# Kernel tuning notes

Measured on AMD Instinct MI355X. Metric: run time of the kernel, lower is better.

## Reference

```python
import jax, jax.numpy as jnp
import numpy as np


def setup_inputs() -> dict:
    key = jax.random.key(0)
    ks = jax.random.split(key, 4)
    B, T, I, H = 64, 1024, 256, 512
    s = 1.0 / np.sqrt(I + H)  # torch Linear default init scale
    xs = jax.random.normal(ks[0], (B, T, I), dtype=jnp.float32)
    Wz = jax.random.uniform(ks[1], (I + H, H), jnp.float32, -s, s)
    Wr = jax.random.uniform(ks[2], (I + H, H), jnp.float32, -s, s)
    Wh = jax.random.uniform(ks[3], (I + H, H), jnp.float32, -s, s)
    bz = jnp.zeros((H,), jnp.float32)
    br = jnp.zeros((H,), jnp.float32)
    bh = jnp.zeros((H,), jnp.float32)
    return {"xs": xs, "Wz": Wz, "bz": bz, "Wr": Wr, "br": br, "Wh": Wh, "bh": bh}


def reference(xs, Wz, bz, Wr, br, Wh, bh):
    B, T, I = xs.shape
    H = Wz.shape[1]
    # split weights into input / hidden blocks so per-step work avoids concat
    Wz_x, Wz_h = Wz[:I], Wz[I:]
    Wr_x, Wr_h = Wr[:I], Wr[I:]
    Wh_x, Wh_h = Wh[:I], Wh[I:]
    # precompute all input projections in one big GEMM per gate: [B,T,H]
    xz = jnp.einsum('bti,ih->bth', xs, Wz_x) + bz
    xr = jnp.einsum('bti,ih->bth', xs, Wr_x) + br
    xh = jnp.einsum('bti,ih->bth', xs, Wh_x) + bh

    def step(h, inp):
        xz_t, xr_t, xh_t = inp
        zt = jax.nn.sigmoid(xz_t + h @ Wz_h)
        rt = jax.nn.sigmoid(xr_t + h @ Wr_h)
        ht = jnp.tanh(xh_t + (rt * h) @ Wh_h)
        h_next = (1 - zt) * h + zt * ht
        return h_next, h_next

    h0 = jnp.zeros((B, H), xs.dtype)
    # scan over time: inputs as [T, B, H]
    xs_t = (jnp.swapaxes(xz, 0, 1), jnp.swapaxes(xr, 0, 1), jnp.swapaxes(xh, 0, 1))
    h_last, hs = jax.lax.scan(step, h0, xs_t)
    return jnp.swapaxes(hs, 0, 1), h_last
```

## Files before the change

### kernel.cpp

```cpp
#include <hip/hip_runtime.h>
#include <cmath>

typedef __bf16 bf16x8 __attribute__((ext_vector_type(8)));
typedef float  f32x4  __attribute__((ext_vector_type(4)));
typedef unsigned int u32;
typedef unsigned long long u64;
typedef u32 u32x4v __attribute__((ext_vector_type(4)));

#define T_STEPS 1024
#define I_DIM   256
#define H_DIM   512
#define B_TOT   64
#define NBT     4
#define NCT     32
#define BT      16
#define CT      16
#define FDOM    64
#define WPB     (H_DIM / 2)
#define LLSZ    (2 * NBT * BT * WPB)

__device__ __forceinline__ f32x4 mfma16(bf16x8 a, bf16x8 b, f32x4 c) {
    return __builtin_amdgcn_mfma_f32_16x16x32_bf16(a, b, c, 0, 0, 0);
}

__device__ __forceinline__ bf16x8 cvt8r(float4 a, float4 b) {
    bf16x8 f;
    f[0] = (__bf16)a.x; f[1] = (__bf16)a.y; f[2] = (__bf16)a.z; f[3] = (__bf16)a.w;
    f[4] = (__bf16)b.x; f[5] = (__bf16)b.y; f[6] = (__bf16)b.z; f[7] = (__bf16)b.w;
    return f;
}

__device__ __forceinline__ int ld_flag(const int* p) {
    return __hip_atomic_load(p, __ATOMIC_RELAXED, __HIP_MEMORY_SCOPE_AGENT);
}
__device__ __forceinline__ void st_flag(int* p, int v) {
    __hip_atomic_store(p, v, __ATOMIC_RELAXED, __HIP_MEMORY_SCOPE_AGENT);
}
__device__ __forceinline__ u64 ld_u64(const u64* p) {
    return __hip_atomic_load(p, __ATOMIC_RELAXED, __HIP_MEMORY_SCOPE_AGENT);
}
__device__ __forceinline__ void st_u64(u64* p, u64 v) {
    __hip_atomic_store(p, v, __ATOMIC_RELAXED, __HIP_MEMORY_SCOPE_AGENT);
}

__device__ __forceinline__ void wait32(const int* fdom, int target) {
    const int* p = fdom + (threadIdx.x & 31);
    for (int g = 0; g < (1 << 22); ++g) {
        int v = ld_flag(p);
        if (__ballot(v >= target) == ~0ull) break;
    }
    asm volatile("" ::: "memory");
}

__device__ __forceinline__ void ll_load16(const u64* b0, const u64* b1,
                                          const u64* b2, const u64* b3,
                                          u32 tag, u64* wrd) {
    for (int g = 0; g < (1 << 20); ++g) {
        #pragma unroll
        for (int k = 0; k < 4; ++k) {
            wrd[0  + k] = ld_u64(b0 + k);
            wrd[4  + k] = ld_u64(b1 + k);
            wrd[8  + k] = ld_u64(b2 + k);
            wrd[12 + k] = ld_u64(b3 + k);
        }
        bool ok = true;
        #pragma unroll
        for (int x = 0; x < 16; ++x) ok &= ((u32)(wrd[x] >> 32) == tag);
        if (__ballot(ok) == ~0ull) break;
        __builtin_amdgcn_s_sleep(2);
    }
}

__device__ __forceinline__ bf16x8 frag_of(const u64* wrd) {
    u32x4v d;
    d.x = (u32)wrd[0]; d.y = (u32)wrd[1]; d.z = (u32)wrd[2]; d.w = (u32)wrd[3];
    return __builtin_bit_cast(bf16x8, d);
}

__global__ __launch_bounds__(256, 1) void gru_persist(
    const float* __restrict__ xs,
    const float* __restrict__ Wz, const float* __restrict__ bz,
    const float* __restrict__ Wr, const float* __restrict__ br,
    const float* __restrict__ Wh, const float* __restrict__ bh,
    float* __restrict__ out,
    u64* hll, u64* rhll, int* flag_h, int* flag_r)
{
    const int bid  = blockIdx.x;
    const int i    = bid & (NBT - 1);
    const int j    = bid >> 2;
    const int tid  = threadIdx.x;
    const int w    = tid >> 6;
    const int lane = tid & 63;
    const int q    = lane >> 4;
    const int ln   = lane & 15;
    const int cb   = j * CT;

    __shared__ float red1[2][4][16][17];
    __shared__ float red2[4][16][17];

    bf16x8 BZ[6], BR[6], BH[6];
    #pragma unroll
    for (int s = 0; s < 6; ++s) {
        int kk = w + 4 * s;
        int krow = kk * 32 + q * 8;
        bf16x8 fz, fr, fh;
        #pragma unroll
        for (int jj = 0; jj < 8; ++jj) {
            int off = (krow + jj) * H_DIM + cb + ln;
            fz[jj] = (__bf16)Wz[off];
            fr[jj] = (__bf16)Wr[off];
            fh[jj] = (__bf16)Wh[off];
        }
        BZ[s] = fz; BR[s] = fr; BH[s] = fh;
    }

    const int m = tid >> 4;
    const int c = tid & 15;
    const float bzc = bz[cb + c], brc = br[cb + c], bhc = bh[cb + c];
    float hprev = 0.0f;

    const float* xrow = xs + (size_t)(i * BT + ln) * T_STEPS * I_DIM;
    int* fh_dom = flag_h + i * FDOM;
    int* fr_dom = flag_r + i * FDOM;
    int* my_fh  = fh_dom + j;
    int* my_fr  = fr_dom + j;

    const int widx = q * 4;

    float4 xr[4];
    {
        const float* x0 = xrow;
        xr[0] = *(const float4*)(x0 + (w    ) * 32 + q * 8);
        xr[1] = *(const float4*)(x0 + (w    ) * 32 + q * 8 + 4);
        xr[2] = *(const float4*)(x0 + (w + 4) * 32 + q * 8);
        xr[3] = *(const float4*)(x0 + (w + 4) * 32 + q * 8 + 4);
    }

    for (int t = 0; t < T_STEPS; ++t) {
        const int p = t & 1, pp = p ^ 1;

        float4 xn[4];
        {
            int tn = (t + 1 < T_STEPS) ? t + 1 : t;
            const float* xp = xrow + (size_t)tn * I_DIM;
            xn[0] = *(const float4*)(xp + (w    ) * 32 + q * 8);
            xn[1] = *(const float4*)(xp + (w    ) * 32 + q * 8 + 4);
            xn[2] = *(const float4*)(xp + (w + 4) * 32 + q * 8);
            xn[3] = *(const float4*)(xp + (w + 4) * 32 + q * 8 + 4);
        }

        f32x4 accz = {0,0,0,0}, accr = {0,0,0,0}, acch = {0,0,0,0};

        {
            bf16x8 ax0 = cvt8r(xr[0], xr[1]);
            bf16x8 ax1 = cvt8r(xr[2], xr[3]);
            accz = mfma16(ax0, BZ[0], accz);
            accr = mfma16(ax0, BR[0], accr);
            acch = mfma16(ax0, BH[0], acch);
            accz = mfma16(ax1, BZ[1], accz);
            accr = mfma16(ax1, BR[1], accr);
            acch = mfma16(ax1, BH[1], acch);
        }

        {
            if (t > 0) wait32(fh_dom, t);
            const u64* hb = hll + ((size_t)((pp * NBT + i) * BT) + ln) * WPB;
            u64 wh[16];
            ll_load16(hb + (w     ) * 16 + widx,
                      hb + (w +  4) * 16 + widx,
                      hb + (w +  8) * 16 + widx,
                      hb + (w + 12) * 16 + widx,
                      (u32)t, wh);
            #pragma unroll
            for (int s = 0; s < 4; ++s) {
                bf16x8 ah = frag_of(&wh[4 * s]);
                accz = mfma16(ah, BZ[s + 2], accz);
                accr = mfma16(ah, BR[s + 2], accr);
            }
        }

        #pragma unroll
        for (int r4 = 0; r4 < 4; ++r4) {
            red1[0][w][q*4 + r4][ln] = accz[r4];
            red1[1][w][q*4 + r4][ln] = accr[r4];
        }
        __syncthreads();

        float zv;
        {
            float pz = red1[0][0][m][c] + red1[0][1][m][c] + red1[0][2][m][c] + red1[0][3][m][c] + bzc;
            float pr = red1[1][0][m][c] + red1[1][1][m][c] + red1[1][2][m][c] + red1[1][3][m][c] + brc;
            zv = 1.0f / (1.0f + __expf(-pz));
            float rv = 1.0f / (1.0f + __expf(-pr));
            unsigned short v16 = __builtin_bit_cast(unsigned short, (__bf16)(rv * hprev));
            unsigned short nb  = (unsigned short)__shfl((int)v16, lane + 1);
            if (!(c & 1)) {
                u64 wrd = (u64)((u32)v16 | ((u32)nb << 16)) | ((u64)(u32)(t + 1) << 32);
                st_u64(rhll + ((size_t)((p * NBT + i) * BT) + m) * WPB + ((cb + c) >> 1), wrd);
            }
            __syncthreads();
            if (tid == 0) st_flag(my_fr, t + 1);
        }

        {
            wait32(fr_dom, t + 1);
            const u64* rb = rhll + ((size_t)((p * NBT + i) * BT) + ln) * WPB;
            u64 wr_[16];
            ll_load16(rb + (w     ) * 16 + widx,
                      rb + (w +  4) * 16 + widx,
                      rb + (w +  8) * 16 + widx,
                      rb + (w + 12) * 16 + widx,
                      (u32)(t + 1), wr_);
            #pragma unroll
            for (int s = 0; s < 4; ++s)
                acch = mfma16(frag_of(&wr_[4 * s]), BH[s + 2], acch);
        }

        #pragma unroll
        for (int r4 = 0; r4 < 4; ++r4)
            red2[w][q*4 + r4][ln] = acch[r4];
        __syncthreads();

        {
            float ph  = red2[0][m][c] + red2[1][m][c] + red2[2][m][c] + red2[3][m][c] + bhc;
            float e2  = __expf(2.0f * ph);
            float htl = (e2 - 1.0f) / (e2 + 1.0f);
            float hn  = (1.0f - zv) * hprev + zv * htl;
            hprev = hn;

            unsigned short v16 = __builtin_bit_cast(unsigned short, (__bf16)hn);
            unsigned short nb  = (unsigned short)__shfl((int)v16, lane + 1);
            if (!(c & 1)) {
                u64 wrd = (u64)((u32)v16 | ((u32)nb << 16)) | ((u64)(u32)(t + 1) << 32);
                st_u64(hll + ((size_t)((p * NBT + i) * BT) + m) * WPB + ((cb + c) >> 1), wrd);
            }
            __syncthreads();
            if (tid == 0) st_flag(my_fh, t + 1);

            int bglob = i * BT + m;
            out[((size_t)bglob * T_STEPS + t) * H_DIM + cb + c] = hn;
            if (t == T_STEPS - 1)
                out[(size_t)B_TOT * T_STEPS * H_DIM + (size_t)bglob * H_DIM + cb + c] = hn;
        }

        xr[0] = xn[0]; xr[1] = xn[1]; xr[2] = xn[2]; xr[3] = xn[3];
    }
}

extern "C" void kernel_launch(void* const* d_in, const int* in_sizes, int n_in,
                              void* d_out, int out_size, void* d_ws, size_t ws_size,
                              hipStream_t stream)
{
    const float* xs = (const float*)d_in[0];
    const float* Wz = (const float*)d_in[1];
    const float* bz = (const float*)d_in[2];
    const float* Wr = (const float*)d_in[3];
    const float* br = (const float*)d_in[4];
    const float* Wh = (const float*)d_in[5];
    const float* bh = (const float*)d_in[6];
    float* out = (float*)d_out;

    u64* hll  = (u64*)d_ws;
    u64* rhll = hll + LLSZ;
    int* flag_h = (int*)((char*)d_ws + 2 * LLSZ * sizeof(u64));
    int* flag_r = flag_h + NBT * FDOM;

    hipMemsetAsync(d_ws, 0, 2 * LLSZ * sizeof(u64) + 2 * NBT * FDOM * sizeof(int), stream);
    gru_persist<<<dim3(NBT * NCT), dim3(256), 0, stream>>>(
        xs, Wz, bz, Wr, br, Wh, bh, out, hll, rhll, flag_h, flag_r);
}
```

Before: 7.277 ms.

## Retile GRU to 8-row batch groups with per-wave flags and sc0 polling

Changes the persistent GRU partition from 4×32 blocks of 16 rows by 16 columns to 8×16 blocks of 8 rows by 32 columns. Each wave now computes two 16-column MFMA tiles, and half of each MFMA's rows are wasted because only 8 batch rows exist. The block-wide barrier before flag publication is replaced by per-wave flags (64 per domain), each set after a vmcnt wait. Flag and data polling first uses sc0 inline-asm loads for a bounded number of tries, then falls back to atomic loads. The goal is lower cross-block synchronization latency on the sequential critical path, at the cost of redundant MFMA work and more flags to poll.

```diff
diff --git a/kernel.cpp b/kernel.cpp
--- a/kernel.cpp
+++ b/kernel.cpp
@@ -11,13 +11,13 @@
 #define I_DIM   256
 #define H_DIM   512
 #define B_TOT   64
-#define NBT     4
-#define NCT     32
-#define BT      16
-#define CT      16
+#define NBT     8
+#define NCT     16
+#define BT      8
+#define CT      32
 #define FDOM    64
 #define WPB     (H_DIM / 2)
-#define LLSZ    (2 * NBT * BT * WPB)
+#define LLW     (2 * NBT * BT * WPB)
 
 __device__ __forceinline__ f32x4 mfma16(bf16x8 a, bf16x8 b, f32x4 c) {
     return __builtin_amdgcn_mfma_f32_16x16x32_bf16(a, b, c, 0, 0, 0);
@@ -43,8 +43,25 @@
     __hip_atomic_store(p, v, __ATOMIC_RELAXED, __HIP_MEMORY_SCOPE_AGENT);
 }
 
-__device__ __forceinline__ void wait32(const int* fdom, int target) {
-    const int* p = fdom + (threadIdx.x & 31);
+__device__ __forceinline__ int ld_flag_sc0(const int* p) {
+    int v;
+    asm volatile("global_load_dword %0, %1, off sc0\n\ts_waitcnt vmcnt(0)"
+                 : "=v"(v) : "v"(p) : "memory");
+    return v;
+}
+__device__ __forceinline__ void ld2_sc0(const u64* p, u64& d) {
+    asm volatile("global_load_dwordx2 %0, %1, off sc0" : "=v"(d) : "v"(p) : "memory");
+}
+
+__device__ __forceinline__ void wait64(const int* fdom, int target, bool& rem) {
+    const int* p = fdom + (threadIdx.x & 63);
+    if (!rem) {
+        for (int g = 0; g < 64; ++g) {
+            int v = ld_flag_sc0(p);
+            if (__ballot(v >= target) == ~0ull) return;
+        }
+        rem = true;
+    }
     for (int g = 0; g < (1 << 22); ++g) {
         int v = ld_flag(p);
         if (__ballot(v >= target) == ~0ull) break;
@@ -52,22 +69,33 @@
     asm volatile("" ::: "memory");
 }
 
-__device__ __forceinline__ void ll_load16(const u64* b0, const u64* b1,
-                                          const u64* b2, const u64* b3,
-                                          u32 tag, u64* wrd) {
-    for (int g = 0; g < (1 << 20); ++g) {
+__device__ __forceinline__ void load16(const u64* base, int w, int q, u32 tag,
+                                       u64* wd, bool& rem) {
+    if (!rem) {
+        for (int r = 0; r < 8; ++r) {
+            #pragma unroll
+            for (int s = 0; s < 4; ++s) {
+                const u64* ptr = base + (w + 4 * s) * 16 + q * 4;
+                ld2_sc0(ptr + 0, wd[4*s+0]);
+                ld2_sc0(ptr + 1, wd[4*s+1]);
+                ld2_sc0(ptr + 2, wd[4*s+2]);
+                ld2_sc0(ptr + 3, wd[4*s+3]);
+            }
+            asm volatile("s_waitcnt vmcnt(0)" ::: "memory");
+            __builtin_amdgcn_sched_barrier(0);
+            bool ok = true;
+            #pragma unroll
+            for (int x = 0; x < 16; ++x) ok &= ((u32)(wd[x] >> 32) == tag);
+            if (__ballot(ok) == ~0ull) return;
+            __builtin_amdgcn_s_sleep(4);
+        }
+        rem = true;
+    }
+    #pragma unroll
+    for (int s = 0; s < 4; ++s) {
+        const u64* ptr = base + (w + 4 * s) * 16 + q * 4;
         #pragma unroll
-        for (int k = 0; k < 4; ++k) {
-            wrd[0  + k] = ld_u64(b0 + k);
-            wrd[4  + k] = ld_u64(b1 + k);
-            wrd[8  + k] = ld_u64(b2 + k);
-            wrd[12 + k] = ld_u64(b3 + k);
-        }
-        bool ok = true;
-        #pragma unroll
-        for (int x = 0; x < 16; ++x) ok &= ((u32)(wrd[x] >> 32) == tag);
-        if (__ballot(ok) == ~0ull) break;
-        __builtin_amdgcn_s_sleep(2);
+        for (int k = 0; k < 4; ++k) wd[4*s+k] = ld_u64(ptr + k);
     }
 }
 
@@ -87,7 +115,7 @@
 {
     const int bid  = blockIdx.x;
     const int i    = bid & (NBT - 1);
-    const int j    = bid >> 2;
+    const int j    = bid >> 3;
     const int tid  = threadIdx.x;
     const int w    = tid >> 6;
     const int lane = tid & 63;
@@ -95,45 +123,45 @@
     const int ln   = lane & 15;
     const int cb   = j * CT;
 
-    __shared__ float red1[2][4][16][17];
-    __shared__ float red2[4][16][17];
-
-    bf16x8 BZ[6], BR[6], BH[6];
+    __shared__ float red1[2][4][8][33];
+    __shared__ float red2[4][8][33];
+
+    bf16x8 WZ[6][2], WR[6][2], WH[6][2];
     #pragma unroll
     for (int s = 0; s < 6; ++s) {
-        int kk = w + 4 * s;
-        int krow = kk * 32 + q * 8;
-        bf16x8 fz, fr, fh;
+        int krow = (w + 4 * s) * 32 + q * 8;
         #pragma unroll
-        for (int jj = 0; jj < 8; ++jj) {
-            int off = (krow + jj) * H_DIM + cb + ln;
-            fz[jj] = (__bf16)Wz[off];
-            fr[jj] = (__bf16)Wr[off];
-            fh[jj] = (__bf16)Wh[off];
-        }
-        BZ[s] = fz; BR[s] = fr; BH[s] = fh;
-    }
-
-    const int m = tid >> 4;
-    const int c = tid & 15;
+        for (int n = 0; n < 2; ++n) {
+            bf16x8 fz, fr, fh;
+            #pragma unroll
+            for (int jj = 0; jj < 8; ++jj) {
+                int off = (krow + jj) * H_DIM + cb + n * 16 + ln;
+                fz[jj] = (__bf16)Wz[off];
+                fr[jj] = (__bf16)Wr[off];
+                fh[jj] = (__bf16)Wh[off];
+            }
+            WZ[s][n] = fz; WR[s][n] = fr; WH[s][n] = fh;
+        }
+    }
+
+    const int m = tid >> 5;
+    const int c = tid & 31;
     const float bzc = bz[cb + c], brc = br[cb + c], bhc = bh[cb + c];
     float hprev = 0.0f;
 
-    const float* xrow = xs + (size_t)(i * BT + ln) * T_STEPS * I_DIM;
+    const float* xrow = xs + (size_t)(i * BT + (ln & 7)) * T_STEPS * I_DIM;
     int* fh_dom = flag_h + i * FDOM;
     int* fr_dom = flag_r + i * FDOM;
-    int* my_fh  = fh_dom + j;
-    int* my_fr  = fr_dom + j;
-
-    const int widx = q * 4;
-
-    float4 xr[4];
+
+    bool remh = false, remr = false;
+
+    float4 xst[4];
     {
         const float* x0 = xrow;
-        xr[0] = *(const float4*)(x0 + (w    ) * 32 + q * 8);
-        xr[1] = *(const float4*)(x0 + (w    ) * 32 + q * 8 + 4);
-        xr[2] = *(const float4*)(x0 + (w + 4) * 32 + q * 8);
-        xr[3] = *(const float4*)(x0 + (w + 4) * 32 + q * 8 + 4);
+        xst[0] = *(const float4*)(x0 + (w    ) * 32 + q * 8);
+        xst[1] = *(const float4*)(x0 + (w    ) * 32 + q * 8 + 4);
+        xst[2] = *(const float4*)(x0 + (w + 4) * 32 + q * 8);
+        xst[3] = *(const float4*)(x0 + (w + 4) * 32 + q * 8 + 4);
     }
 
     for (int t = 0; t < T_STEPS; ++t) {
@@ -149,40 +177,48 @@
             xn[3] = *(const float4*)(xp + (w + 4) * 32 + q * 8 + 4);
         }
 
-        f32x4 accz = {0,0,0,0}, accr = {0,0,0,0}, acch = {0,0,0,0};
-
-        {
-            bf16x8 ax0 = cvt8r(xr[0], xr[1]);
-            bf16x8 ax1 = cvt8r(xr[2], xr[3]);
-            accz = mfma16(ax0, BZ[0], accz);
-            accr = mfma16(ax0, BR[0], accr);
-            acch = mfma16(ax0, BH[0], acch);
-            accz = mfma16(ax1, BZ[1], accz);
-            accr = mfma16(ax1, BR[1], accr);
-            acch = mfma16(ax1, BH[1], acch);
-        }
-
-        {
-            if (t > 0) wait32(fh_dom, t);
-            const u64* hb = hll + ((size_t)((pp * NBT + i) * BT) + ln) * WPB;
-            u64 wh[16];
-            ll_load16(hb + (w     ) * 16 + widx,
-                      hb + (w +  4) * 16 + widx,
-                      hb + (w +  8) * 16 + widx,
-                      hb + (w + 12) * 16 + widx,
-                      (u32)t, wh);
+        f32x4 accz[2] = {{0,0,0,0},{0,0,0,0}};
+        f32x4 accr[2] = {{0,0,0,0},{0,0,0,0}};
+        f32x4 acch[2] = {{0,0,0,0},{0,0,0,0}};
+
+        {
+            bf16x8 ax0 = cvt8r(xst[0], xst[1]);
+            bf16x8 ax1 = cvt8r(xst[2], xst[3]);
+            #pragma unroll
+            for (int n = 0; n < 2; ++n) {
+                accz[n] = mfma16(ax0, WZ[0][n], accz[n]);
+                accr[n] = mfma16(ax0, WR[0][n], accr[n]);
+                acch[n] = mfma16(ax0, WH[0][n], acch[n]);
+                accz[n] = mfma16(ax1, WZ[1][n], accz[n]);
+                accr[n] = mfma16(ax1, WR[1][n], accr[n]);
+                acch[n] = mfma16(ax1, WH[1][n], acch[n]);
+            }
+        }
+
+        {
+            wait64(fh_dom, t, remh);
+            const u64* hb = hll + ((size_t)((pp * NBT + i) * BT) + (ln & 7)) * WPB;
+            u64 wd[16];
+            load16(hb, w, q, (u32)t, wd, remh);
             #pragma unroll
             for (int s = 0; s < 4; ++s) {
-                bf16x8 ah = frag_of(&wh[4 * s]);
-                accz = mfma16(ah, BZ[s + 2], accz);
-                accr = mfma16(ah, BR[s + 2], accr);
-            }
-        }
-
-        #pragma unroll
-        for (int r4 = 0; r4 < 4; ++r4) {
-            red1[0][w][q*4 + r4][ln] = accz[r4];
-            red1[1][w][q*4 + r4][ln] = accr[r4];
+                bf16x8 ah = frag_of(&wd[4 * s]);
+                #pragma unroll
+                for (int n = 0; n < 2; ++n) {
+                    accz[n] = mfma16(ah, WZ[s + 2][n], accz[n]);
+                    accr[n] = mfma16(ah, WR[s + 2][n], accr[n]);
+                }
+            }
+        }
+
+        if (q < 2) {
+            #pragma unroll
+            for (int n = 0; n < 2; ++n)
+                #pragma unroll
+                for (int r4 = 0; r4 < 4; ++r4) {
+                    red1[0][w][q * 4 + r4][n * 16 + ln] = accz[n][r4];
+                    red1[1][w][q * 4 + r4][n * 16 + ln] = accr[n][r4];
+                }
         }
         __syncthreads();
 
@@ -198,27 +234,31 @@
                 u64 wrd = (u64)((u32)v16 | ((u32)nb << 16)) | ((u64)(u32)(t + 1) << 32);
                 st_u64(rhll + ((size_t)((p * NBT + i) * BT) + m) * WPB + ((cb + c) >> 1), wrd);
             }
-            __syncthreads();
-            if (tid == 0) st_flag(my_fr, t + 1);
-        }
-
-        {
-            wait32(fr_dom, t + 1);
-            const u64* rb = rhll + ((size_t)((p * NBT + i) * BT) + ln) * WPB;
-            u64 wr_[16];
-            ll_load16(rb + (w     ) * 16 + widx,
-                      rb + (w +  4) * 16 + widx,
-                      rb + (w +  8) * 16 + widx,
-                      rb + (w + 12) * 16 + widx,
-                      (u32)(t + 1), wr_);
-            #pragma unroll
-            for (int s = 0; s < 4; ++s)
-                acch = mfma16(frag_of(&wr_[4 * s]), BH[s + 2], acch);
-        }
-
-        #pragma unroll
-        for (int r4 = 0; r4 < 4; ++r4)
-            red2[w][q*4 + r4][ln] = acch[r4];
+            asm volatile("s_waitcnt vmcnt(0)" ::: "memory");
+            if (lane == 0) st_flag(fr_dom + j * 4 + w, t + 1);
+        }
+
+        {
+            wait64(fr_dom, t + 1, remr);
+            const u64* rb = rhll + ((size_t)((p * NBT + i) * BT) + (ln & 7)) * WPB;
+            u64 we[16];
+            load16(rb, w, q, (u32)(t + 1), we, remr);
+            #pragma unroll
+            for (int s = 0; s < 4; ++s) {
+                bf16x8 ar_ = frag_of(&we[4 * s]);
+                #pragma unroll
+                for (int n = 0; n < 2; ++n)
+                    acch[n] = mfma16(ar_, WH[s + 2][n], acch[n]);
+            }
+        }
+
+        if (q < 2) {
+            #pragma unroll
+            for (int n = 0; n < 2; ++n)
+                #pragma unroll
+                for (int r4 = 0; r4 < 4; ++r4)
+                    red2[w][q * 4 + r4][n * 16 + ln] = acch[n][r4];
+        }
         __syncthreads();
 
         {
@@ -234,8 +274,8 @@
                 u64 wrd = (u64)((u32)v16 | ((u32)nb << 16)) | ((u64)(u32)(t + 1) << 32);
                 st_u64(hll + ((size_t)((p * NBT + i) * BT) + m) * WPB + ((cb + c) >> 1), wrd);
             }
-            __syncthreads();
-            if (tid == 0) st_flag(my_fh, t + 1);
+            asm volatile("s_waitcnt vmcnt(0)" ::: "memory");
+            if (lane == 0) st_flag(fh_dom + j * 4 + w, t + 1);
 
             int bglob = i * BT + m;
             out[((size_t)bglob * T_STEPS + t) * H_DIM + cb + c] = hn;
@@ -243,7 +283,7 @@
                 out[(size_t)B_TOT * T_STEPS * H_DIM + (size_t)bglob * H_DIM + cb + c] = hn;
         }
 
-        xr[0] = xn[0]; xr[1] = xn[1]; xr[2] = xn[2]; xr[3] = xn[3];
+        xst[0] = xn[0]; xst[1] = xn[1]; xst[2] = xn[2]; xst[3] = xn[3];
     }
 }
 
@@ -261,11 +301,11 @@
     float* out = (float*)d_out;
 
     u64* hll  = (u64*)d_ws;
-    u64* rhll = hll + LLSZ;
-    int* flag_h = (int*)((char*)d_ws + 2 * LLSZ * sizeof(u64));
+    u64* rhll = hll + LLW;
+    int* flag_h = (int*)((char*)d_ws + 2 * LLW * sizeof(u64));
     int* flag_r = flag_h + NBT * FDOM;
 
-    hipMemsetAsync(d_ws, 0, 2 * LLSZ * sizeof(u64) + 2 * NBT * FDOM * sizeof(int), stream);
+    hipMemsetAsync(d_ws, 0, 2 * LLW * sizeof(u64) + 2 * NBT * FDOM * sizeof(int), stream);
     gru_persist<<<dim3(NBT * NCT), dim3(256), 0, stream>>>(
         xs, Wz, bz, Wr, br, Wh, bh, out, hll, rhll, flag_h, flag_r);
 }
```

Result: slower. 10.65 ms (+46.4%).
